# Performance work log

Hardware: AMD Instinct MI355X
Metric: run time of the kernel (lower is better)

Reference implementation:

```python
import jax, jax.numpy as jnp
from jax import lax
import numpy as np

N_CLUSTERS = 8
G_CLUSTERS = 2
D_DIM = 512
DN = ('NCHW', 'OIHW', 'NCHW')


def _conv(x, w, b):
    y = lax.conv_general_dilated(x, w, window_strides=(1, 1), padding='VALID',
                                 dimension_numbers=DN)
    return y + b[None, :, None, None]


def setup_inputs() -> dict:
    key = jax.random.key(0)
    ks = jax.random.split(key, 6)
    B, D, H, W = 32, D_DIM, 7, 250
    KG = N_CLUSTERS + G_CLUSTERS
    scale = 1.0 / np.sqrt(D * 7)
    return {
        'x': jax.random.normal(ks[0], (B, D, H, W), dtype=jnp.float32),
        'feat_w': jax.random.normal(ks[1], (D, D, 7, 1), dtype=jnp.float32) * scale,
        'feat_b': jax.random.normal(ks[2], (D,), dtype=jnp.float32) * 0.01,
        'assign_w': jax.random.normal(ks[3], (KG, D, 7, 1), dtype=jnp.float32) * scale,
        'assign_b': jax.random.normal(ks[4], (KG,), dtype=jnp.float32) * 0.01,
        'centroids': jax.random.uniform(ks[5], (D, KG), dtype=jnp.float32),
    }


def reference(x, feat_w, feat_b, assign_w, assign_b, centroids):
    # features branch: conv(7,1) + ReLU -> (B, D, H', W)
    feat = jnp.maximum(_conv(x, feat_w, feat_b), 0.0)
    # assignment branch: conv(7,1) -> softmax over clusters -> (B, K+G, H', W)
    soft = jax.nn.softmax(_conv(x, assign_w, assign_b), axis=1)
    # Fused VLAD aggregation (mathematically identical to
    # sum_hw soft[b,k,hw] * (feat[b,d,hw] - centroids[d,k]) without
    # materializing the (B,D,K+G,H',W) residual tensor):
    s_sum = soft.sum(axis=(-2, -1))                                # (B, K+G)
    agg = jnp.einsum('bkhw,bdhw->bdk', soft, feat)                 # (B, D, K+G)
    cluster_res = agg - centroids[None, :, :] * s_sum[:, None, :]  # (B, D, K+G)
    cluster_res = cluster_res[..., :N_CLUSTERS]                    # drop ghost clusters
    # L2 normalize over feature dim (torch F.normalize, eps=1e-12)
    norm = jnp.sqrt(jnp.sum(cluster_res * cluster_res, axis=1, keepdims=True))
    cluster_l2 = cluster_res / jnp.maximum(norm, 1e-12)
    # (B, D, K) -> (B, K, D) -> (B, K*D)
    out = jnp.swapaxes(cluster_l2, 1, 2).reshape(x.shape[0], N_CLUSTERS * D_DIM)
    return out
```

## Files before the change

kernel.cpp:

```cpp
#include <hip/hip_runtime.h>
#include <stdint.h>

typedef float f32x4 __attribute__((ext_vector_type(4)));
typedef __bf16 bf16x8 __attribute__((ext_vector_type(8)));
typedef unsigned short ushortx8 __attribute__((ext_vector_type(8)));

#define D_DIM 512
#define KGC 10
#define NCLU 8
#define BATCH 32
#define WPOS 250
#define WPAD 256
#define KDIM 3584
#define MROWS 522
#define MPAD 528
#define MBIG 640
#define BM 160
#define BN 64
#define NS 56
#define NTB 128
#define MSB 4

__device__ __forceinline__ float bf2f(unsigned short u) {
  union { unsigned int i; float f; } v; v.i = ((unsigned int)u) << 16; return v.f;
}
__device__ __forceinline__ unsigned short f2bf(float f) {
  union { float f; unsigned int i; } v; v.f = f;
  unsigned int r = v.i + 0x7FFFu + ((v.i >> 16) & 1u);
  return (unsigned short)(r >> 16);
}

__device__ __forceinline__ void load_lds16(const void* g, void* l) {
  __builtin_amdgcn_global_load_lds(
      (const __attribute__((address_space(1))) void*)g,
      (__attribute__((address_space(3))) void*)l, 16, 0, 0);
}

__global__ void prep_kernel(const float* __restrict__ fw,
                            const float* __restrict__ fb,
                            const float* __restrict__ aw,
                            const float* __restrict__ ab,
                            unsigned short* __restrict__ Wcat,
                            float* __restrict__ bcat) {
  int r = blockIdx.x;
  unsigned short* dst = Wcat + (size_t)r * KDIM;
  const float* src = (r < D_DIM) ? (fw + (size_t)r * KDIM)
                   : (r < MROWS) ? (aw + (size_t)(r - D_DIM) * KDIM)
                                 : nullptr;
  for (int i = threadIdx.x; i < KDIM / 4; i += 256) {
    unsigned short o0 = 0, o1 = 0, o2 = 0, o3 = 0;
    if (src) {
      float4 v = ((const float4*)src)[i];
      o0 = f2bf(v.x); o1 = f2bf(v.y); o2 = f2bf(v.z); o3 = f2bf(v.w);
    }
    ushort4 o; o.x = o0; o.y = o1; o.z = o2; o.w = o3;
    ((ushort4*)dst)[i] = o;
  }
  if (threadIdx.x == 0)
    bcat[r] = r < D_DIM ? fb[r] : (r < MROWS ? ab[r - D_DIM] : 0.f);
}

__global__ __launch_bounds__(256, 2) void gemm_fused(
    const float* __restrict__ x, const unsigned short* __restrict__ Wcat,
    const float* __restrict__ bcat, unsigned short* __restrict__ Y) {
  __shared__ __align__(16) unsigned short Wl[BM * 64];
  __shared__ __align__(16) unsigned short Xl[BN * 64];
  const int tid = threadIdx.x;
  const int hw = blockIdx.x;
  const int work = (hw & 7) * 64 + (hw >> 3);
  const int nt = work >> 2, ms = work & 3;
  const int lane = tid & 63, wv = tid >> 6;
  const int wm = wv >> 1, wn = wv & 1;
  const int fr = lane & 15, kg = lane >> 4;
  const int sx = fr & 7;
  const int nloc = tid & 63, oc = tid >> 6;
  const int nglob = nt * BN + nloc;
  const int b = nglob >> 8, ncol = nglob & 255;
  const bool okn = ncol < WPOS;
  const float* xb = x + (size_t)b * KDIM * WPOS + ncol;
  const unsigned short* Wg = Wcat + (size_t)ms * BM * KDIM;

  float xr[16];
  auto loadx = [&](int st) {
#pragma unroll
    for (int pass = 0; pass < 2; pass++) {
      int k0 = st * 64 + (oc + 4 * pass) * 8;
#pragma unroll
      for (int e = 0; e < 8; e++)
        xr[pass * 8 + e] = okn ? xb[(size_t)(k0 + e) * WPOS] : 0.f;
    }
  };

  f32x4 acc[5][2];
  const f32x4 zero = {0.f, 0.f, 0.f, 0.f};
#pragma unroll
  for (int f = 0; f < 5; f++) { acc[f][0] = zero; acc[f][1] = zero; }

  loadx(0);

  for (int st = 0; st < NS; st++) {
    __syncthreads();
#pragma unroll
    for (int it = 0; it < 5; it++) {
      int s = it * 256 + tid;
      int row = s >> 3, p = s & 7;
      int blk = p ^ (row & 7);
      load_lds16(Wg + (size_t)row * KDIM + st * 64 + blk * 8, &Wl[s * 8]);
    }
#pragma unroll
    for (int pass = 0; pass < 2; pass++) {
      int oct = oc + 4 * pass;
      ushortx8 pk;
#pragma unroll
      for (int e = 0; e < 8; e++) pk[e] = f2bf(xr[pass * 8 + e]);
      *(ushortx8*)&Xl[nloc * 64 + (oct ^ (nloc & 7)) * 8] = pk;
    }
    __syncthreads();
    if (st + 1 < NS) loadx(st + 1);
#pragma unroll
    for (int ks = 0; ks < 2; ks++) {
      const int off = ((ks * 4 + kg) ^ sx) * 8;
      bf16x8 b0 = *(const bf16x8*)&Xl[(wn * 32 + fr) * 64 + off];
      bf16x8 b1 = *(const bf16x8*)&Xl[(wn * 32 + 16 + fr) * 64 + off];
#pragma unroll
      for (int f = 0; f < 5; f++) {
        bf16x8 af = *(const bf16x8*)&Wl[(wm * 80 + f * 16 + fr) * 64 + off];
        acc[f][0] = __builtin_amdgcn_mfma_f32_16x16x32_bf16(af, b0, acc[f][0], 0, 0, 0);
        acc[f][1] = __builtin_amdgcn_mfma_f32_16x16x32_bf16(af, b1, acc[f][1], 0, 0, 0);
      }
    }
  }

  const int bb = (nt * BN) >> 8;
  const int cbase = (nt * BN) & 255;
  unsigned short* Yb = Y + (size_t)bb * MPAD * WPAD;
#pragma unroll
  for (int f = 0; f < 5; f++) {
    const int m0 = ms * BM + wm * 80 + f * 16 + kg * 4;
#pragma unroll
    for (int nf = 0; nf < 2; nf++) {
      const int c = cbase + wn * 32 + nf * 16 + fr;
#pragma unroll
      for (int r = 0; r < 4; r++) {
        const int m = m0 + r;
        if (m < MPAD) {
          float v = acc[f][nf][r] + bcat[m];
          if (m < D_DIM) v = fmaxf(v, 0.f);
          Yb[(size_t)m * WPAD + c] = f2bf(v);
        }
      }
    }
  }
}

__global__ __launch_bounds__(256) void epi_kernel(
    const unsigned short* __restrict__ Y, const float* __restrict__ cent,
    float* __restrict__ out) {
  __shared__ float soft[WPAD];
  __shared__ float red[4];
  const int b = blockIdx.x >> 3, k = blockIdx.x & 7;
  const int tid = threadIdx.x;
  const unsigned short* Yb = Y + (size_t)b * MPAD * WPAD;

  float sv = 0.f;
  if (tid < WPOS) {
    float lg[KGC];
    float mx = -1e30f;
#pragma unroll
    for (int j = 0; j < KGC; j++) {
      lg[j] = bf2f(Yb[(size_t)(D_DIM + j) * WPAD + tid]);
      mx = fmaxf(mx, lg[j]);
    }
    float s = 0.f, ek = 0.f;
#pragma unroll
    for (int j = 0; j < KGC; j++) {
      float e = __expf(lg[j] - mx);
      s += e;
      if (j == k) ek = e;
    }
    sv = ek / s;
  }
  soft[tid] = sv;
  __syncthreads();

  float v = sv;
#pragma unroll
  for (int o = 32; o > 0; o >>= 1) v += __shfl_down(v, o, 64);
  if ((tid & 63) == 0) red[tid >> 6] = v;
  __syncthreads();
  float ssum = red[0] + red[1] + red[2] + red[3];

  float a0 = 0.f, a1 = 0.f;
  const unsigned short* row0 = Yb + (size_t)tid * WPAD;
  const unsigned short* row1 = Yb + (size_t)(tid + 256) * WPAD;
  for (int w = 0; w < WPAD; w += 8) {
    ushortx8 f0 = *(const ushortx8*)(row0 + w);
    ushortx8 f1 = *(const ushortx8*)(row1 + w);
#pragma unroll
    for (int u = 0; u < 8; u++) {
      float s = soft[w + u];
      a0 += bf2f(f0[u]) * s;
      a1 += bf2f(f1[u]) * s;
    }
  }
  float c0 = a0 - cent[(size_t)tid * KGC + k] * ssum;
  float c1 = a1 - cent[(size_t)(tid + 256) * KGC + k] * ssum;

  __syncthreads();
  float q = c0 * c0 + c1 * c1;
#pragma unroll
  for (int o = 32; o > 0; o >>= 1) q += __shfl_down(q, o, 64);
  if ((tid & 63) == 0) red[tid >> 6] = q;
  __syncthreads();
  float norm = sqrtf(red[0] + red[1] + red[2] + red[3]);
  float inv = 1.f / fmaxf(norm, 1e-12f);

  float* ob = out + (size_t)b * (NCLU * D_DIM) + (size_t)k * D_DIM;
  ob[tid] = c0 * inv;
  ob[tid + 256] = c1 * inv;
}

extern "C" void kernel_launch(void* const* d_in, const int* in_sizes, int n_in,
                              void* d_out, int out_size, void* d_ws, size_t ws_size,
                              hipStream_t stream) {
  const float* x  = (const float*)d_in[0];
  const float* fw = (const float*)d_in[1];
  const float* fb = (const float*)d_in[2];
  const float* aw = (const float*)d_in[3];
  const float* ab = (const float*)d_in[4];
  const float* ce = (const float*)d_in[5];
  float* out = (float*)d_out;
  char* ws = (char*)d_ws;

  const size_t WC_BYTES = (size_t)MBIG * KDIM * 2;
  const size_t BC_BYTES = 4096;
  unsigned short* Wc = (unsigned short*)(ws);
  float*          bc = (float*)(ws + WC_BYTES);
  unsigned short* Yv = (unsigned short*)(ws + WC_BYTES + BC_BYTES);

  prep_kernel<<<MBIG, 256, 0, stream>>>(fw, fb, aw, ab, Wc, bc);
  gemm_fused<<<NTB * MSB, 256, 0, stream>>>(x, Wc, bc, Yv);
  epi_kernel<<<BATCH * NCLU, 256, 0, stream>>>(Yv, ce, out);
}
```

Baseline: 268.2 us.

## Double-buffer LDS tiles in GEMM and widen epilogue to 512 threads

The GEMM main loop now uses two LDS buffers for the weight and input tiles. The next stage's weights are staged and its inputs converted while MFMA runs on the current buffer, which drops one barrier per k-step. The epilogue kernel switches to 512 threads with one feature row per thread and eight independent accumulators, giving more parallelism and shorter dependency chains. LDS use per GEMM block doubles (about 52KB), which may limit occupancy.

```diff
diff --git a/kernel.cpp b/kernel.cpp
--- a/kernel.cpp
+++ b/kernel.cpp
@@ -63,8 +63,8 @@
 __global__ __launch_bounds__(256, 2) void gemm_fused(
     const float* __restrict__ x, const unsigned short* __restrict__ Wcat,
     const float* __restrict__ bcat, unsigned short* __restrict__ Y) {
-  __shared__ __align__(16) unsigned short Wl[BM * 64];
-  __shared__ __align__(16) unsigned short Xl[BN * 64];
+  __shared__ __align__(16) unsigned short Wl[2][BM * 64];
+  __shared__ __align__(16) unsigned short Xl[2][BN * 64];
   const int tid = threadIdx.x;
   const int hw = blockIdx.x;
   const int work = (hw & 7) * 64 + (hw >> 3);
@@ -90,45 +90,57 @@
         xr[pass * 8 + e] = okn ? xb[(size_t)(k0 + e) * WPOS] : 0.f;
     }
   };
-
-  f32x4 acc[5][2];
-  const f32x4 zero = {0.f, 0.f, 0.f, 0.f};
-#pragma unroll
-  for (int f = 0; f < 5; f++) { acc[f][0] = zero; acc[f][1] = zero; }
-
-  loadx(0);
-
-  for (int st = 0; st < NS; st++) {
-    __syncthreads();
+  auto stageW = [&](int st, int buf) {
 #pragma unroll
     for (int it = 0; it < 5; it++) {
       int s = it * 256 + tid;
       int row = s >> 3, p = s & 7;
       int blk = p ^ (row & 7);
-      load_lds16(Wg + (size_t)row * KDIM + st * 64 + blk * 8, &Wl[s * 8]);
-    }
+      load_lds16(Wg + (size_t)row * KDIM + st * 64 + blk * 8, &Wl[buf][s * 8]);
+    }
+  };
+  auto writeX = [&](int buf) {
 #pragma unroll
     for (int pass = 0; pass < 2; pass++) {
       int oct = oc + 4 * pass;
       ushortx8 pk;
 #pragma unroll
       for (int e = 0; e < 8; e++) pk[e] = f2bf(xr[pass * 8 + e]);
-      *(ushortx8*)&Xl[nloc * 64 + (oct ^ (nloc & 7)) * 8] = pk;
-    }
-    __syncthreads();
-    if (st + 1 < NS) loadx(st + 1);
+      *(ushortx8*)&Xl[buf][nloc * 64 + (oct ^ (nloc & 7)) * 8] = pk;
+    }
+  };
+
+  f32x4 acc[5][2];
+  const f32x4 zero = {0.f, 0.f, 0.f, 0.f};
+#pragma unroll
+  for (int f = 0; f < 5; f++) { acc[f][0] = zero; acc[f][1] = zero; }
+
+  stageW(0, 0);
+  loadx(0);
+  writeX(0);
+  loadx(1);
+  __syncthreads();
+
+  for (int st = 0; st < NS; st++) {
+    const int cur = st & 1, nxt = cur ^ 1;
+    if (st + 1 < NS) {
+      stageW(st + 1, nxt);
+      writeX(nxt);
+    }
+    if (st + 2 < NS) loadx(st + 2);
 #pragma unroll
     for (int ks = 0; ks < 2; ks++) {
       const int off = ((ks * 4 + kg) ^ sx) * 8;
-      bf16x8 b0 = *(const bf16x8*)&Xl[(wn * 32 + fr) * 64 + off];
-      bf16x8 b1 = *(const bf16x8*)&Xl[(wn * 32 + 16 + fr) * 64 + off];
+      bf16x8 b0 = *(const bf16x8*)&Xl[cur][(wn * 32 + fr) * 64 + off];
+      bf16x8 b1 = *(const bf16x8*)&Xl[cur][(wn * 32 + 16 + fr) * 64 + off];
 #pragma unroll
       for (int f = 0; f < 5; f++) {
-        bf16x8 af = *(const bf16x8*)&Wl[(wm * 80 + f * 16 + fr) * 64 + off];
+        bf16x8 af = *(const bf16x8*)&Wl[cur][(wm * 80 + f * 16 + fr) * 64 + off];
         acc[f][0] = __builtin_amdgcn_mfma_f32_16x16x32_bf16(af, b0, acc[f][0], 0, 0, 0);
         acc[f][1] = __builtin_amdgcn_mfma_f32_16x16x32_bf16(af, b1, acc[f][1], 0, 0, 0);
       }
     }
+    __syncthreads();
   }
 
   const int bb = (nt * BN) >> 8;
@@ -153,11 +165,11 @@
   }
 }
 
-__global__ __launch_bounds__(256) void epi_kernel(
+__global__ __launch_bounds__(512) void epi_kernel(
     const unsigned short* __restrict__ Y, const float* __restrict__ cent,
     float* __restrict__ out) {
   __shared__ float soft[WPAD];
-  __shared__ float red[4];
+  __shared__ float red[8];
   const int b = blockIdx.x >> 3, k = blockIdx.x & 7;
   const int tid = threadIdx.x;
   const unsigned short* Yb = Y + (size_t)b * MPAD * WPAD;
@@ -180,7 +192,7 @@
     }
     sv = ek / s;
   }
-  soft[tid] = sv;
+  if (tid < WPAD) soft[tid] = sv;
   __syncthreads();
 
   float v = sv;
@@ -188,36 +200,44 @@
   for (int o = 32; o > 0; o >>= 1) v += __shfl_down(v, o, 64);
   if ((tid & 63) == 0) red[tid >> 6] = v;
   __syncthreads();
-  float ssum = red[0] + red[1] + red[2] + red[3];
-
-  float a0 = 0.f, a1 = 0.f;
-  const unsigned short* row0 = Yb + (size_t)tid * WPAD;
-  const unsigned short* row1 = Yb + (size_t)(tid + 256) * WPAD;
+  float ssum = 0.f;
+#pragma unroll
+  for (int i = 0; i < 8; i++) ssum += red[i];
+
+  float a[8];
+#pragma unroll
+  for (int u = 0; u < 8; u++) a[u] = 0.f;
+  const unsigned short* row = Yb + (size_t)tid * WPAD;
   for (int w = 0; w < WPAD; w += 8) {
-    ushortx8 f0 = *(const ushortx8*)(row0 + w);
-    ushortx8 f1 = *(const ushortx8*)(row1 + w);
-#pragma unroll
-    for (int u = 0; u < 8; u++) {
-      float s = soft[w + u];
-      a0 += bf2f(f0[u]) * s;
-      a1 += bf2f(f1[u]) * s;
-    }
-  }
-  float c0 = a0 - cent[(size_t)tid * KGC + k] * ssum;
-  float c1 = a1 - cent[(size_t)(tid + 256) * KGC + k] * ssum;
-
-  __syncthreads();
-  float q = c0 * c0 + c1 * c1;
+    ushortx8 f0 = *(const ushortx8*)(row + w);
+    float4 s0 = *(const float4*)&soft[w];
+    float4 s1 = *(const float4*)&soft[w + 4];
+    a[0] += bf2f(f0[0]) * s0.x;
+    a[1] += bf2f(f0[1]) * s0.y;
+    a[2] += bf2f(f0[2]) * s0.z;
+    a[3] += bf2f(f0[3]) * s0.w;
+    a[4] += bf2f(f0[4]) * s1.x;
+    a[5] += bf2f(f0[5]) * s1.y;
+    a[6] += bf2f(f0[6]) * s1.z;
+    a[7] += bf2f(f0[7]) * s1.w;
+  }
+  float asum = ((a[0] + a[1]) + (a[2] + a[3])) + ((a[4] + a[5]) + (a[6] + a[7]));
+  float c = asum - cent[(size_t)tid * KGC + k] * ssum;
+
+  __syncthreads();
+  float q = c * c;
 #pragma unroll
   for (int o = 32; o > 0; o >>= 1) q += __shfl_down(q, o, 64);
   if ((tid & 63) == 0) red[tid >> 6] = q;
   __syncthreads();
-  float norm = sqrtf(red[0] + red[1] + red[2] + red[3]);
+  float nsum = 0.f;
+#pragma unroll
+  for (int i = 0; i < 8; i++) nsum += red[i];
+  float norm = sqrtf(nsum);
   float inv = 1.f / fmaxf(norm, 1e-12f);
 
   float* ob = out + (size_t)b * (NCLU * D_DIM) + (size_t)k * D_DIM;
-  ob[tid] = c0 * inv;
-  ob[tid + 256] = c1 * inv;
+  ob[tid] = c * inv;
 }
 
 extern "C" void kernel_launch(void* const* d_in, const int* in_sizes, int n_in,
@@ -240,5 +260,5 @@
 
   prep_kernel<<<MBIG, 256, 0, stream>>>(fw, fb, aw, ab, Wc, bc);
   gemm_fused<<<NTB * MSB, 256, 0, stream>>>(x, Wc, bc, Yv);
-  epi_kernel<<<BATCH * NCLU, 256, 0, stream>>>(Yv, ce, out);
-}
+  epi_kernel<<<BATCH * NCLU, 512, 0, stream>>>(Yv, ce, out);
+}
```

Result: slower. 285.4 us (+6.4%).
